# Performance work log

Hardware: AMD Instinct MI355X
Metric: run time of the kernel (lower is better)

## Reference

```python
import jax, jax.numpy as jnp
import numpy as np

H = 64
L = 3
NG = 1024
# node types: 0 user, 1 card, 2 transaction, 3 merchant, 4 location, 5 device
N_NODES = [100000, 150000, 500000, 20000, 5000, 50000]
N_TX = N_NODES[2]
FEAT_DIMS = [8, 6, 12, 6, 5, 5]
NAMES = ["user", "card", "transaction", "merchant", "location", "device"]
# relation r -> (src_type, dst_type); order matches the HeteroConv dict:
# owns, made, at, in, using, followed_by, owned_by, made_with, receives, has, used_in, preceded
REL = [(0, 1), (1, 2), (2, 3), (2, 4), (2, 5), (2, 2), (1, 0), (2, 1), (3, 2), (4, 2), (5, 2), (2, 2)]
E_CNT = [150000, 500000, 500000, 500000, 500000, 500000, 150000, 500000, 500000, 500000, 500000, 500000]


def gat_conv(x_src, x_dst, src, dst, W, a_s, a_d, b, n_dst):
    # PyG GATConv, heads=1, shared src/dst linear (int in_channels), no self-loops (bipartite hetero)
    xs = x_src @ W  # [Ns, H]
    xd = x_dst @ W  # [Nd, H]
    e = jax.nn.leaky_relu((xs @ a_s)[src] + (xd @ a_d)[dst], 0.2)  # [E]
    m = jax.ops.segment_max(e, dst, num_segments=n_dst)
    m = jnp.where(jnp.isfinite(m), m, 0.0)
    p = jnp.exp(e - m[dst])
    s = jax.ops.segment_sum(p, dst, num_segments=n_dst)
    alpha = p / (s[dst] + 1e-16)
    out = jax.ops.segment_sum(alpha[:, None] * xs[src], dst, num_segments=n_dst)
    return out + b


def setup_inputs():
    key = jax.random.key(0)
    ks = iter(jax.random.split(key, 80))
    inp = {}
    for n, d, nm in zip(N_NODES, FEAT_DIMS, NAMES):
        inp["x_" + nm] = jax.random.normal(next(ks), (n, d), jnp.float32)
    for d, nm in zip(FEAT_DIMS, NAMES):
        inp["emb_" + nm + "_W"] = (jax.random.normal(next(ks), (d, H), jnp.float32) / np.sqrt(d)).astype(jnp.float32)
        inp["emb_" + nm + "_b"] = jnp.zeros((H,), jnp.float32)
    inp["gat_W"] = (jax.random.normal(next(ks), (L, 12, H, H), jnp.float32) / np.sqrt(H)).astype(jnp.float32)
    inp["gat_a_src"] = jax.random.normal(next(ks), (L, 12, H), jnp.float32) * 0.1
    inp["gat_a_dst"] = jax.random.normal(next(ks), (L, 12, H), jnp.float32) * 0.1
    inp["gat_b"] = jnp.zeros((L, 12, H), jnp.float32)
    inp["pool_W"] = (jax.random.normal(next(ks), (2 * H, H), jnp.float32) / np.sqrt(2 * H)).astype(jnp.float32)
    inp["pool_b"] = jnp.zeros((H,), jnp.float32)
    inp["cls_W1"] = (jax.random.normal(next(ks), (H, H), jnp.float32) / np.sqrt(H)).astype(jnp.float32)
    inp["cls_b1"] = jnp.zeros((H,), jnp.float32)
    inp["cls_W2"] = (jax.random.normal(next(ks), (H, 1), jnp.float32) / np.sqrt(H)).astype(jnp.float32)
    inp["cls_b2"] = jnp.zeros((1,), jnp.float32)
    for r, (s, d) in enumerate(REL):
        inp[f"e{r}_src"] = jax.random.randint(next(ks), (E_CNT[r],), 0, N_NODES[s])
        inp[f"e{r}_dst"] = jax.random.randint(next(ks), (E_CNT[r],), 0, N_NODES[d])
    inp["batch"] = jnp.sort(jax.random.randint(next(ks), (N_TX,), 0, NG))
    return inp


def reference(x_user, x_card, x_transaction, x_merchant, x_location, x_device,
              emb_user_W, emb_user_b, emb_card_W, emb_card_b,
              emb_transaction_W, emb_transaction_b, emb_merchant_W, emb_merchant_b,
              emb_location_W, emb_location_b, emb_device_W, emb_device_b,
              gat_W, gat_a_src, gat_a_dst, gat_b,
              pool_W, pool_b, cls_W1, cls_b1, cls_W2, cls_b2,
              e0_src, e0_dst, e1_src, e1_dst, e2_src, e2_dst, e3_src, e3_dst,
              e4_src, e4_dst, e5_src, e5_dst, e6_src, e6_dst, e7_src, e7_dst,
              e8_src, e8_dst, e9_src, e9_dst, e10_src, e10_dst, e11_src, e11_dst,
              batch):
    edges = [(e0_src, e0_dst), (e1_src, e1_dst), (e2_src, e2_dst), (e3_src, e3_dst),
             (e4_src, e4_dst), (e5_src, e5_dst), (e6_src, e6_dst), (e7_src, e7_dst),
             (e8_src, e8_dst), (e9_src, e9_dst), (e10_src, e10_dst), (e11_src, e11_dst)]
    x = [x_user @ emb_user_W + emb_user_b,
         x_card @ emb_card_W + emb_card_b,
         x_transaction @ emb_transaction_W + emb_transaction_b,
         x_merchant @ emb_merchant_W + emb_merchant_b,
         x_location @ emb_location_W + emb_location_b,
         x_device @ emb_device_W + emb_device_b]
    for l in range(L):
        agg = [jnp.zeros((n, H), x[0].dtype) for n in N_NODES]
        for r, (s, d) in enumerate(REL):  # HeteroConv default aggr='sum'
            agg[d] = agg[d] + gat_conv(x[s], x[d], edges[r][0], edges[r][1],
                                       gat_W[l, r], gat_a_src[l, r], gat_a_dst[l, r],
                                       gat_b[l, r], N_NODES[d])
        x = [jax.nn.relu(a) for a in agg]  # dropout(p=0.2) is identity in eval mode
    tx = x[2]
    cnt = jax.ops.segment_sum(jnp.ones((N_TX,), tx.dtype), batch, num_segments=NG)
    mean_pool = jax.ops.segment_sum(tx, batch, num_segments=NG) / jnp.maximum(cnt, 1.0)[:, None]
    max_pool = jax.ops.segment_max(tx, batch, num_segments=NG)
    max_pool = jnp.where(jnp.isfinite(max_pool), max_pool, 0.0)
    pooled = jnp.concatenate([mean_pool, max_pool], axis=1) @ pool_W + pool_b
    h = jax.nn.relu(tx @ cls_W1 + cls_b1)
    fraud_scores = jax.nn.sigmoid(h @ cls_W2 + cls_b2)
    return fraud_scores, pooled
```

## Files before the change

### kernel.cpp

```cpp
#include <hip/hip_runtime.h>
#include <hip/hip_bf16.h>

typedef unsigned int u32;
typedef unsigned short u16;
typedef _Float16 f16;
typedef float f32x4 __attribute__((ext_vector_type(4)));
typedef short bf16x8 __attribute__((ext_vector_type(8)));

#define CDIV(a,b) (((a)+(b)-1)/(b))

__device__ __forceinline__ float bf2f(u32 h){ return __uint_as_float(h<<16); }
__device__ __forceinline__ u16 f2bf(float f){
  u32 u=__float_as_uint(f);
  return (u16)((u + 0x7fffu + ((u>>16)&1u))>>16);
}
__device__ __forceinline__ void unpack8(const u16* p, float* xr){
  uint4 v=*(const uint4*)p;
  xr[0]=bf2f(v.x&0xffffu); xr[1]=bf2f(v.x>>16);
  xr[2]=bf2f(v.y&0xffffu); xr[3]=bf2f(v.y>>16);
  xr[4]=bf2f(v.z&0xffffu); xr[5]=bf2f(v.z>>16);
  xr[6]=bf2f(v.w&0xffffu); xr[7]=bf2f(v.w>>16);
}
__device__ __forceinline__ int iclamp(int i, int n){
  unsigned u=(unsigned)i; return (u>=(unsigned)n)?0:i;
}

struct EdgeTab {
  const int* dst[12];
  const int* src[12];
  int seo[13];
  int rpo[13];
  int nd[12];
  int ns[12];
};

struct GTab {
  int nn[6]; int xo[6];
  int rst[12];
  int aso[12], ado[12], rpo[12], seo[12];
  int tord[6]; int bofs[7];
  int abofs[7];
  int nrel[6], rel[6][6];
  int nrole[6]; int rwv[6][12]; int rofs[6][12];
  int dszb;
};

__global__ void kdiag(float* out, int n, float v){
  int i=blockIdx.x*blockDim.x+threadIdx.x;
  if(i<n) out[i]=(i==0)?v:0.f;
}
__global__ void kzeroi(int* p, int n){
  int i=blockIdx.x*blockDim.x+threadIdx.x;
  if(i<n) p[i]=0;
}
__global__ void kbsum(const float* __restrict__ gb, float* __restrict__ bsum){
  int l=blockIdx.x/6, t=blockIdx.x%6, j=threadIdx.x;
  const int rd[12]={1,2,3,4,5,2,0,1,2,2,2,2};
  float a=0.f;
  #pragma unroll
  for(int r=0;r<12;++r) if(rd[r]==t) a += gb[(l*12+r)*64 + j];
  bsum[(l*6+t)*64 + j]=a;
}
__global__ void kwconv(const float* __restrict__ gw, u16* __restrict__ wt, int total){
  int o=blockIdx.x*blockDim.x+threadIdx.x;
  if(o>=total) return;
  int m=o>>12, rem=o&4095, j=rem>>6, k=rem&63;
  wt[o]=f2bf(gw[(m<<12)+(k<<6)+j]);
}
__global__ void kwv(const float* __restrict__ gw, const float* __restrict__ gas,
                    const float* __restrict__ gad, float* __restrict__ wv){
  int m=blockIdx.x;
  int lr=m>>1, role=m&1;
  int k=threadIdx.x;
  const float* a=(role?gad:gas)+(size_t)lr*64;
  const float* W=gw+(size_t)lr*4096;
  float acc=0.f;
  for(int j=0;j<64;++j) acc += W[k*64+j]*a[j];
  wv[(size_t)m*64+k]=acc;
}

__global__ void khistC(EdgeTab et, int* __restrict__ RP, int Etot, int c0, int c1){
  int i=blockIdx.x*blockDim.x+threadIdx.x;
  if(i>=Etot) return;
  int r=0;
  #pragma unroll
  for(int k=1;k<12;++k) r += (i>=et.seo[k]) ? 1 : 0;
  int e=i-et.seo[r];
  int rpidx=et.rpo[r]+iclamp(et.dst[r][e], et.nd[r]);
  if(rpidx>=c0 && rpidx<c1) atomicAdd(RP+rpidx,1);
}
__global__ void kscan1(const int* __restrict__ hist, int* __restrict__ rp, int* __restrict__ bsum, int N){
  __shared__ int lds[256];
  __shared__ int pref[256];
  int b=blockIdx.x, t=threadIdx.x;
  int base=b*4096+t*16;
  int v[16]; int s=0;
  #pragma unroll
  for(int k=0;k<16;++k){ int idx=base+k; v[k]=(idx<N)?hist[idx]:0; s+=v[k]; }
  lds[t]=s; __syncthreads();
  if(t==0){ int run=0; for(int i=0;i<256;++i){ pref[i]=run; run+=lds[i]; } bsum[b]=run; }
  __syncthreads();
  int run=pref[t];
  #pragma unroll
  for(int k=0;k<16;++k){ int idx=base+k; if(idx<N) rp[idx]=run; run+=v[k]; }
}
__global__ void kscan2b(int* bsum, int nb){
  __shared__ int lds[256], pref[256], tot;
  int t=threadIdx.x;
  int v[4]; int s=0;
  #pragma unroll
  for(int k=0;k<4;++k){ int idx=t*4+k; v[k]=(idx<nb)?bsum[idx]:0; s+=v[k]; }
  lds[t]=s; __syncthreads();
  if(t==0){ int run=0; for(int i=0;i<256;++i){ pref[i]=run; run+=lds[i]; } tot=run; }
  __syncthreads();
  int run=pref[t];
  #pragma unroll
  for(int k=0;k<4;++k){ int idx=t*4+k; if(idx<nb){ int x=v[k]; bsum[idx]=run; run+=x; } }
  if(t==0) bsum[nb]=tot;
}
__global__ void kscan3(int* __restrict__ rp, const int* __restrict__ bsum, int N){
  int i=blockIdx.x*blockDim.x+threadIdx.x;
  if(i<N) rp[i]+=bsum[i>>12];
}
__global__ void kscatterC(EdgeTab et, int* __restrict__ RP, int* __restrict__ SRCS,
                          int Etot, int c0, int c1){
  int i=blockIdx.x*blockDim.x+threadIdx.x;
  if(i>=Etot) return;
  int r=0;
  #pragma unroll
  for(int k=1;k<12;++k) r += (i>=et.seo[k]) ? 1 : 0;
  int e=i-et.seo[r];
  int rpidx=et.rpo[r]+iclamp(et.dst[r][e], et.nd[r]);
  if(rpidx>=c0 && rpidx<c1){
    int pos=atomicAdd(RP+rpidx,1);
    SRCS[pos]=iclamp(et.src[r][e], et.ns[r]);
  }
}

template<int D>
__global__ void kemb(const float* __restrict__ xin, const float* __restrict__ W,
                     const float* __restrict__ b, u16* __restrict__ xout, int N,
                     const float* __restrict__ WV0, f16* __restrict__ AA, GTab tab, int t){
  int n=blockIdx.x*blockDim.x+threadIdx.x;
  if(n>=N) return;
  float xr[D];
  #pragma unroll
  for(int k=0;k<D;++k) xr[k]=xin[(long)n*D+k];
  float o[64];
  u16* orow=xout+(long)n*64;
  #pragma unroll
  for(int j0=0;j0<64;j0+=8){
    #pragma unroll
    for(int jj=0;jj<8;++jj){
      float a=b[j0+jj];
      #pragma unroll
      for(int k=0;k<D;++k) a += xr[k]*W[k*64+j0+jj];
      o[j0+jj]=a;
    }
    uint4 pk;
    pk.x=(u32)f2bf(o[j0+0])|((u32)f2bf(o[j0+1])<<16);
    pk.y=(u32)f2bf(o[j0+2])|((u32)f2bf(o[j0+3])<<16);
    pk.z=(u32)f2bf(o[j0+4])|((u32)f2bf(o[j0+5])<<16);
    pk.w=(u32)f2bf(o[j0+6])|((u32)f2bf(o[j0+7])<<16);
    *(uint4*)(orow+j0)=pk;
  }
  int nr=tab.nrole[t];
  for(int ro=0;ro<nr;++ro){
    const float* wv=WV0+(size_t)tab.rwv[t][ro]*64;
    float acc=0.f;
    #pragma unroll
    for(int k=0;k<64;++k) acc += o[k]*wv[k];
    AA[tab.rofs[t][ro]+n]=(f16)acc;
  }
}

__global__ void kalphaM(const u16* __restrict__ X, const float* __restrict__ WVl,
                        f16* __restrict__ AA, GTab tab){
  __shared__ float wv[12*64];
  int b=blockIdx.x, tid=threadIdx.x;
  int ti=0;
  #pragma unroll
  for(int k=1;k<6;++k) ti += (b>=tab.abofs[k]) ? 1 : 0;
  int t=tab.tord[ti];
  int nr=tab.nrole[t];
  for(int i=tid;i<nr*64;i+=256){
    int ro=i>>6, j=i&63;
    wv[i]=WVl[tab.rwv[t][ro]*64+j];
  }
  __syncthreads();
  int nid=(b-tab.abofs[ti])*256+tid;
  if(nid>=tab.nn[t]) return;
  const u16* row=X+((long)tab.xo[t]+nid)*64;
  float xr[64];
  #pragma unroll
  for(int j=0;j<64;j+=8) unpack8(row+j,xr+j);
  for(int ro=0;ro<nr;++ro){
    float acc=0.f;
    #pragma unroll
    for(int k=0;k<64;++k) acc += xr[k]*wv[ro*64+k];
    AA[tab.rofs[t][ro]+nid]=(f16)acc;
  }
}

#define LZ 0
#define LW 8192
__global__ void kfusedM2(const u16* __restrict__ Xc, u16* __restrict__ Xn,
                         const u16* __restrict__ WTl, const f16* __restrict__ AA,
                         const int* __restrict__ RP, const int* __restrict__ SRCS,
                         const float* __restrict__ BSl, GTab tab){
  __shared__ char L[16384];
  int tid=threadIdx.x;
  int b=blockIdx.x;
  int ti=0;
  #pragma unroll
  for(int k=1;k<6;++k) ti += (b>=tab.bofs[k]) ? 1 : 0;
  int t=tab.tord[ti];
  int d0=(b-tab.bofs[ti])*64;
  int Nt=tab.nn[t];
  int nid=tid>>2, q=tid&3;
  int d=d0+nid;

  f32x4 acc[4];
  #pragma unroll
  for(int ct=0;ct<4;++ct){ acc[ct][0]=0.f; acc[ct][1]=0.f; acc[ct][2]=0.f; acc[ct][3]=0.f; }

  int nrel=tab.nrel[t];
  for(int ri=0;ri<nrel;++ri){
    int r=tab.rel[t][ri];
    __syncthreads();
    {
      const uint4* s4=(const uint4*)(WTl+(size_t)r*4096);
      uint4 v0=s4[tid*2], v1=s4[tid*2+1];
      int b0=tid*32, j=b0>>7;
      *(uint4*)(L+LW+((b0   )^((j&7)<<4)))=v0;
      *(uint4*)(L+LW+((b0+16)^((j&7)<<4)))=v1;
    }
    float z[16];
    #pragma unroll
    for(int k=0;k<16;++k) z[k]=0.f;
    float sden=0.f;
    if(d<Nt){
      int b1=RP[tab.rpo[r]+d];
      int b0e= d? RP[tab.rpo[r]+d-1] : tab.seo[r];
      float adv=(float)AA[tab.dszb+tab.ado[r]+d];
      const u16* xbase=Xc+(long)tab.xo[tab.rst[r]]*64;
      const f16* asp=AA+tab.aso[r];
      float m=-3.4e38f;
      for(int e=b0e;e<b1;++e){
        float ev=(float)asp[SRCS[e]]+adv;
        ev = ev>=0.f?ev:0.2f*ev;
        m=fmaxf(m,ev);
      }
      int e=b0e;
      for(; e+1<b1; e+=2){
        int sr0=SRCS[e], sr1=SRCS[e+1];
        float ev0=(float)asp[sr0]+adv; ev0 = ev0>=0.f?ev0:0.2f*ev0;
        float ev1=(float)asp[sr1]+adv; ev1 = ev1>=0.f?ev1:0.2f*ev1;
        float p0=__expf(ev0-m), p1=__expf(ev1-m);
        const u16* rw0=xbase+(long)sr0*64+q*16;
        const u16* rw1=xbase+(long)sr1*64+q*16;
        uint4 a0=*(const uint4*)rw0;
        uint4 a1=*(const uint4*)(rw0+8);
        uint4 c0=*(const uint4*)rw1;
        uint4 c1=*(const uint4*)(rw1+8);
        sden+=p0+p1;
        float xr[8];
        unpack8((const u16*)&a0,xr);
        #pragma unroll
        for(int k=0;k<8;++k) z[k]+=p0*xr[k];
        unpack8((const u16*)&a1,xr);
        #pragma unroll
        for(int k=0;k<8;++k) z[8+k]+=p0*xr[k];
        unpack8((const u16*)&c0,xr);
        #pragma unroll
        for(int k=0;k<8;++k) z[k]+=p1*xr[k];
        unpack8((const u16*)&c1,xr);
        #pragma unroll
        for(int k=0;k<8;++k) z[8+k]+=p1*xr[k];
      }
      if(e<b1){
        int sr0=SRCS[e];
        float ev0=(float)asp[sr0]+adv; ev0 = ev0>=0.f?ev0:0.2f*ev0;
        float p0=__expf(ev0-m);
        const u16* rw0=xbase+(long)sr0*64+q*16;
        uint4 a0=*(const uint4*)rw0;
        uint4 a1=*(const uint4*)(rw0+8);
        sden+=p0;
        float xr[8];
        unpack8((const u16*)&a0,xr);
        #pragma unroll
        for(int k=0;k<8;++k) z[k]+=p0*xr[k];
        unpack8((const u16*)&a1,xr);
        #pragma unroll
        for(int k=0;k<8;++k) z[8+k]+=p0*xr[k];
      }
    }
    float inv=1.f/(sden+1e-16f);
    {
      uint4 p0,p1;
      p0.x=(u32)f2bf(z[0]*inv) |((u32)f2bf(z[1]*inv)<<16);
      p0.y=(u32)f2bf(z[2]*inv) |((u32)f2bf(z[3]*inv)<<16);
      p0.z=(u32)f2bf(z[4]*inv) |((u32)f2bf(z[5]*inv)<<16);
      p0.w=(u32)f2bf(z[6]*inv) |((u32)f2bf(z[7]*inv)<<16);
      p1.x=(u32)f2bf(z[8]*inv) |((u32)f2bf(z[9]*inv)<<16);
      p1.y=(u32)f2bf(z[10]*inv)|((u32)f2bf(z[11]*inv)<<16);
      p1.z=(u32)f2bf(z[12]*inv)|((u32)f2bf(z[13]*inv)<<16);
      p1.w=(u32)f2bf(z[14]*inv)|((u32)f2bf(z[15]*inv)<<16);
      int zb=nid*128+q*32;
      *(uint4*)(L+LZ+((zb   )^((nid&7)<<4)))=p0;
      *(uint4*)(L+LZ+((zb+16)^((nid&7)<<4)))=p1;
    }
    __syncthreads();
    {
      int w=tid>>6, l=tid&63;
      int nt=w*16;
      int arow=nt+(l&15);
      int kb=(l>>4)*8;
      #pragma unroll
      for(int ks=0;ks<64;ks+=32){
        int ab=arow*128+(ks+kb)*2;
        uint4 av=*(uint4*)(L+LZ+(ab^((arow&7)<<4)));
        bf16x8 af=*(bf16x8*)&av;
        #pragma unroll
        for(int ct=0;ct<4;++ct){
          int jrow=ct*16+(l&15);
          int bb=jrow*128+(ks+kb)*2;
          uint4 bv=*(uint4*)(L+LW+(bb^((jrow&7)<<4)));
          bf16x8 bfr=*(bf16x8*)&bv;
          acc[ct]=__builtin_amdgcn_mfma_f32_16x16x32_bf16(af,bfr,acc[ct],0,0,0);
        }
      }
    }
  }
  __syncthreads();
  {
    int w=tid>>6, l=tid&63;
    int nt=w*16;
    #pragma unroll
    for(int ct=0;ct<4;++ct){
      #pragma unroll
      for(int r4=0;r4<4;++r4){
        int crow=nt+(l>>4)*4+r4;
        int ccol=ct*16+(l&15);
        int cb=crow*256+ccol*4;
        *(float*)(L+(cb^((crow&7)<<4)))=acc[ct][r4];
      }
    }
  }
  __syncthreads();
  {
    int nn=tid>>2, cq=tid&3;
    if(d0+nn<Nt){
      float cv[16];
      #pragma unroll
      for(int p=0;p<4;++p){
        int cb=nn*256+cq*64+p*16;
        uint4 v=*(uint4*)(L+(cb^((nn&7)<<4)));
        const float* f=(const float*)&v;
        cv[p*4+0]=f[0]; cv[p*4+1]=f[1]; cv[p*4+2]=f[2]; cv[p*4+3]=f[3];
      }
      const float* bs=BSl+t*64+cq*16;
      u32 wd[8];
      #pragma unroll
      for(int i=0;i<8;++i){
        float lo=fmaxf(cv[2*i]  +bs[2*i],  0.f);
        float hi=fmaxf(cv[2*i+1]+bs[2*i+1],0.f);
        wd[i]=(u32)f2bf(lo)|((u32)f2bf(hi)<<16);
      }
      u16* orow=Xn+((long)tab.xo[t]+d0+nn)*64+cq*16;
      uint4 s0; s0.x=wd[0]; s0.y=wd[1]; s0.z=wd[2]; s0.w=wd[3];
      uint4 s1; s1.x=wd[4]; s1.y=wd[5]; s1.z=wd[6]; s1.w=wd[7];
      *(uint4*)orow=s0;
      *(uint4*)(orow+8)=s1;
    }
  }
}

__global__ void kcls(const u16* __restrict__ tx, const float* __restrict__ W1,
                     const float* __restrict__ b1, const float* __restrict__ W2,
                     const float* __restrict__ b2, float* __restrict__ out, int N){
  int n=blockIdx.x*blockDim.x+threadIdx.x;
  if(n>=N) return;
  const u16* row=tx+(long)n*64;
  float xr[64];
  #pragma unroll
  for(int j=0;j<64;j+=8) unpack8(row+j,xr+j);
  float acc2=0.f;
  for(int j=0;j<64;++j){
    float a=b1[j];
    #pragma unroll
    for(int k=0;k<64;++k) a += xr[k]*W1[k*64+j];
    a=fmaxf(a,0.f);
    acc2 += a*W2[j];
  }
  float zv=acc2+b2[0];
  out[n]=1.f/(1.f+__expf(-zv));
}

__global__ void kgrp(const int* __restrict__ batch, int* __restrict__ grp, int N){
  int g=blockIdx.x*blockDim.x+threadIdx.x;
  if(g>1024) return;
  if(g==1024){ grp[1024]=N; return; }
  int lo=0, hi=N;
  while(lo<hi){ int mid=(lo+hi)>>1; if(batch[mid]<g) lo=mid+1; else hi=mid; }
  grp[g]=lo;
}
__global__ void kpoolf(const u16* __restrict__ tx, const int* __restrict__ grp,
                       const float* __restrict__ pW, const float* __restrict__ pb,
                       float* __restrict__ out){
  __shared__ float S[256], M[256], V[128];
  int g=blockIdx.x, t=threadIdx.x, w=t>>6, j=t&63;
  int n0=grp[g], n1=grp[g+1];
  float s=0.f, m=-3.4e38f;
  for(int n=n0+w; n<n1; n+=4){
    float v=bf2f(tx[(long)n*64+j]);
    s+=v; m=fmaxf(m,v);
  }
  S[t]=s; M[t]=m; __syncthreads();
  if(t<64){
    float ss=S[t]+S[t+64]+S[t+128]+S[t+192];
    float mm=fmaxf(fmaxf(M[t],M[t+64]),fmaxf(M[t+128],M[t+192]));
    int cnt=n1-n0;
    V[t]=ss/fmaxf((float)cnt,1.f);
    V[64+t]=(cnt>0)?mm:0.f;
  }
  __syncthreads();
  if(t<64){
    float acc=pb[t];
    for(int k=0;k<128;++k) acc+=V[k]*pW[k*64+t];
    out[(long)g*64+t]=acc;
  }
}

extern "C" void kernel_launch(void* const* d_in, const int* in_sizes, int n_in,
                              void* d_out, int out_size, void* d_ws, size_t ws_size,
                              hipStream_t stream){
  const int   NN[6]={100000,150000,500000,20000,5000,50000};
  const long  XO[6]={0,100000,250000,750000,770000,775000};
  const int   RS[12]={0,1,2,2,2,2,1,2,3,4,5,2};
  const int   RD[12]={1,2,3,4,5,2,0,1,2,2,2,2};
  const int   EC[12]={150000,500000,500000,500000,500000,500000,150000,500000,500000,500000,500000,500000};

  const float* xin[6];  for(int t=0;t<6;++t) xin[t]=(const float*)d_in[t];
  const float* embW[6]; const float* embB[6];
  for(int t=0;t<6;++t){ embW[t]=(const float*)d_in[6+2*t]; embB[t]=(const float*)d_in[7+2*t]; }
  const float* gatW =(const float*)d_in[18];
  const float* gatAs=(const float*)d_in[19];
  const float* gatAd=(const float*)d_in[20];
  const float* gatB =(const float*)d_in[21];
  const float* poolW=(const float*)d_in[22];
  const float* poolB=(const float*)d_in[23];
  const float* W1=(const float*)d_in[24];
  const float* b1=(const float*)d_in[25];
  const float* W2=(const float*)d_in[26];
  const float* b2=(const float*)d_in[27];
  const int* esrc[12]; const int* edst[12];
  for(int r=0;r<12;++r){ esrc[r]=(const int*)d_in[28+2*r]; edst[r]=(const int*)d_in[29+2*r]; }
  const int* batch=(const int*)d_in[52];
  float* out=(float*)d_out;
  (void)in_sizes; (void)n_in;

  EdgeTab et;
  GTab tab;
  int rpo=0, seo=0, asz=0, dsz=0;
  for(int r=0;r<12;++r){
    et.dst[r]=edst[r]; et.src[r]=esrc[r];
    et.seo[r]=seo; et.rpo[r]=rpo;
    et.nd[r]=NN[RD[r]]; et.ns[r]=NN[RS[r]];
    tab.rst[r]=RS[r];
    tab.seo[r]=seo; tab.rpo[r]=rpo;
    tab.aso[r]=asz; tab.ado[r]=dsz;
    seo+=EC[r]; rpo+=NN[RD[r]]+1;
    asz+=NN[RS[r]]; dsz+=NN[RD[r]];
  }
  et.seo[12]=seo; et.rpo[12]=rpo;
  const int Etot=seo;
  const int RPtot=rpo;
  tab.dszb=asz;
  for(int t=0;t<6;++t){ tab.nn[t]=NN[t]; tab.xo[t]=(int)XO[t]; }
  const int TORD[6]={4,3,5,2,1,0};
  int bo=0, abo=0;
  for(int i=0;i<6;++i){
    int t=TORD[i];
    tab.tord[i]=t;
    tab.bofs[i]=bo;   bo+=CDIV(NN[t],64);
    tab.abofs[i]=abo; abo+=CDIV(NN[t],256);
  }
  tab.bofs[6]=bo; tab.abofs[6]=abo;
  for(int t=0;t<6;++t){ tab.nrel[t]=0; tab.nrole[t]=0; }
  for(int r=0;r<12;++r){
    int dt=RD[r];
    tab.rel[dt][tab.nrel[dt]++]=r;
    int st=RS[r];
    tab.rwv[st][tab.nrole[st]]=r*2+0;   tab.rofs[st][tab.nrole[st]++]=tab.aso[r];
    tab.rwv[dt][tab.nrole[dt]]=r*2+1;   tab.rofs[dt][tab.nrole[dt]++]=asz+tab.ado[r];
  }

  char* w=(char*)d_ws;
  size_t off=0;
  auto take=[&](size_t bytes)->void*{
    void* p=w+off; off+=(bytes+(size_t)255)&~(size_t)255; return p;
  };
  u16*   X1   =(u16*)  take(105600000);
  u16*   X2   =(u16*)  take(105600000);
  int*   RP   =(int*)  take((size_t)RPtot*4);
  int*   SRCS =(int*)  take((size_t)Etot*4);
  int*   BS   =(int*)  take(4096);
  f16*   AA   =(f16*)  take((size_t)(asz+dsz)*2);
  float* WV   =(float*)take(72*64*4);
  float* BSUM =(float*)take(4608);
  int*   GRP  =(int*)  take(4104);
  u16*   WT   =(u16*)  take(294912);
  size_t need=off;

  const int B=256;

  if(ws_size<need){
    kdiag<<<CDIV(out_size,B),B,0,stream>>>(out,out_size,(float)(ws_size>>20));
    return;
  }

  kwconv<<<CDIV(147456,B),B,0,stream>>>(gatW,WT,147456);
  kwv<<<72,64,0,stream>>>(gatW,gatAs,gatAd,WV);
  kbsum<<<18,64,0,stream>>>(gatB,BSUM);

  const int NCH=8;
  int CS=CDIV(RPtot,NCH);
  kzeroi<<<CDIV(RPtot,B),B,0,stream>>>(RP,RPtot);
  for(int c=0;c<NCH;++c){
    int c0=c*CS, c1=min(RPtot,c0+CS);
    khistC<<<CDIV(Etot,B),B,0,stream>>>(et,RP,Etot,c0,c1);
  }
  int nbs=CDIV(RPtot,4096);
  kscan1<<<nbs,256,0,stream>>>(RP,RP,BS,RPtot);
  kscan2b<<<1,256,0,stream>>>(BS,nbs);
  kscan3<<<CDIV(RPtot,B),B,0,stream>>>(RP,BS,RPtot);
  for(int c=0;c<NCH;++c){
    int c0=c*CS, c1=min(RPtot,c0+CS);
    kscatterC<<<CDIV(Etot,B),B,0,stream>>>(et,RP,SRCS,Etot,c0,c1);
  }

  kemb< 8><<<CDIV(NN[0],B),B,0,stream>>>(xin[0],embW[0],embB[0],X1+XO[0]*64,NN[0],WV,AA,tab,0);
  kemb< 6><<<CDIV(NN[1],B),B,0,stream>>>(xin[1],embW[1],embB[1],X1+XO[1]*64,NN[1],WV,AA,tab,1);
  kemb<12><<<CDIV(NN[2],B),B,0,stream>>>(xin[2],embW[2],embB[2],X1+XO[2]*64,NN[2],WV,AA,tab,2);
  kemb< 6><<<CDIV(NN[3],B),B,0,stream>>>(xin[3],embW[3],embB[3],X1+XO[3]*64,NN[3],WV,AA,tab,3);
  kemb< 5><<<CDIV(NN[4],B),B,0,stream>>>(xin[4],embW[4],embB[4],X1+XO[4]*64,NN[4],WV,AA,tab,4);
  kemb< 5><<<CDIV(NN[5],B),B,0,stream>>>(xin[5],embW[5],embB[5],X1+XO[5]*64,NN[5],WV,AA,tab,5);

  u16* Xc=X1; u16* Xn=X2;
  for(int l=0;l<3;++l){
    if(l>0) kalphaM<<<abo,256,0,stream>>>(Xc,WV+(size_t)l*1536,AA,tab);
    kfusedM2<<<bo,256,0,stream>>>(Xc,Xn,WT+(size_t)l*49152,AA,RP,SRCS,
                                  BSUM+(size_t)l*384,tab);
    u16* tmp=Xc; Xc=Xn; Xn=tmp;
  }

  kcls<<<CDIV(NN[2],B),B,0,stream>>>(Xc+XO[2]*64,W1,b1,W2,b2,out,NN[2]);

  kgrp<<<CDIV(1025,B),B,0,stream>>>(batch,GRP,NN[2]);
  kpoolf<<<1024,256,0,stream>>>(Xc+XO[2]*64,GRP,poolW,poolB,out+500000);
}
```

Before: 2.506 ms.

## Replace per-destination softmax max pass with a global per-relation upper bound

The GAT softmax no longer scans each destination's edges once just to find the max logit. Instead, kemb and kalphaM use wave reductions and atomicMax on order-preserving encoded floats to record the global max of the source and destination attention terms per relation. kfusedM2 turns the sum of those two maxima into a shared shift through leaky-ReLU. This removes one gather pass over SRCS and the attention array per relation, at the cost of a few extra atomics. Because softmax is shift-invariant the result is mathematically unchanged, but if logits span a wide range, exp could underflow for destinations whose logits sit far below the global bound.

```diff
diff --git a/kernel.cpp b/kernel.cpp
--- a/kernel.cpp
+++ b/kernel.cpp
@@ -13,6 +13,14 @@
 __device__ __forceinline__ u16 f2bf(float f){
   u32 u=__float_as_uint(f);
   return (u16)((u + 0x7fffu + ((u>>16)&1u))>>16);
+}
+__device__ __forceinline__ u32 fenc(float f){
+  u32 u=__float_as_uint(f);
+  return (u&0x80000000u)?~u:(u|0x80000000u);
+}
+__device__ __forceinline__ float fdec2(u32 e){
+  u32 u=(e&0x80000000u)?(e&0x7fffffffu):~e;
+  return __uint_as_float(u);
 }
 __device__ __forceinline__ void unpack8(const u16* p, float* xr){
   uint4 v=*(const uint4*)p;
@@ -140,14 +148,15 @@
 template<int D>
 __global__ void kemb(const float* __restrict__ xin, const float* __restrict__ W,
                      const float* __restrict__ b, u16* __restrict__ xout, int N,
-                     const float* __restrict__ WV0, f16* __restrict__ AA, GTab tab, int t){
+                     const float* __restrict__ WV0, f16* __restrict__ AA,
+                     u32* __restrict__ MG0, GTab tab, int t){
   int n=blockIdx.x*blockDim.x+threadIdx.x;
-  if(n>=N) return;
+  bool valid=(n<N);
+  int nc=valid?n:0;
   float xr[D];
   #pragma unroll
-  for(int k=0;k<D;++k) xr[k]=xin[(long)n*D+k];
+  for(int k=0;k<D;++k) xr[k]=xin[(long)nc*D+k];
   float o[64];
-  u16* orow=xout+(long)n*64;
   #pragma unroll
   for(int j0=0;j0<64;j0+=8){
     #pragma unroll
@@ -157,12 +166,14 @@
       for(int k=0;k<D;++k) a += xr[k]*W[k*64+j0+jj];
       o[j0+jj]=a;
     }
-    uint4 pk;
-    pk.x=(u32)f2bf(o[j0+0])|((u32)f2bf(o[j0+1])<<16);
-    pk.y=(u32)f2bf(o[j0+2])|((u32)f2bf(o[j0+3])<<16);
-    pk.z=(u32)f2bf(o[j0+4])|((u32)f2bf(o[j0+5])<<16);
-    pk.w=(u32)f2bf(o[j0+6])|((u32)f2bf(o[j0+7])<<16);
-    *(uint4*)(orow+j0)=pk;
+    if(valid){
+      uint4 pk;
+      pk.x=(u32)f2bf(o[j0+0])|((u32)f2bf(o[j0+1])<<16);
+      pk.y=(u32)f2bf(o[j0+2])|((u32)f2bf(o[j0+3])<<16);
+      pk.z=(u32)f2bf(o[j0+4])|((u32)f2bf(o[j0+5])<<16);
+      pk.w=(u32)f2bf(o[j0+6])|((u32)f2bf(o[j0+7])<<16);
+      *(uint4*)(xout+(long)n*64+j0)=pk;
+    }
   }
   int nr=tab.nrole[t];
   for(int ro=0;ro<nr;++ro){
@@ -170,12 +181,16 @@
     float acc=0.f;
     #pragma unroll
     for(int k=0;k<64;++k) acc += o[k]*wv[k];
-    AA[tab.rofs[t][ro]+n]=(f16)acc;
+    if(valid) AA[tab.rofs[t][ro]+n]=(f16)acc;
+    float mx=valid?acc:-3.4e38f;
+    #pragma unroll
+    for(int off=32;off;off>>=1) mx=fmaxf(mx,__shfl_xor(mx,off));
+    if((threadIdx.x&63)==0) atomicMax(MG0+tab.rwv[t][ro],fenc(mx));
   }
 }
 
 __global__ void kalphaM(const u16* __restrict__ X, const float* __restrict__ WVl,
-                        f16* __restrict__ AA, GTab tab){
+                        f16* __restrict__ AA, u32* __restrict__ MGl, GTab tab){
   __shared__ float wv[12*64];
   int b=blockIdx.x, tid=threadIdx.x;
   int ti=0;
@@ -189,8 +204,9 @@
   }
   __syncthreads();
   int nid=(b-tab.abofs[ti])*256+tid;
-  if(nid>=tab.nn[t]) return;
-  const u16* row=X+((long)tab.xo[t]+nid)*64;
+  bool valid=(nid<tab.nn[t]);
+  int nc=valid?nid:0;
+  const u16* row=X+((long)tab.xo[t]+nc)*64;
   float xr[64];
   #pragma unroll
   for(int j=0;j<64;j+=8) unpack8(row+j,xr+j);
@@ -198,7 +214,11 @@
     float acc=0.f;
     #pragma unroll
     for(int k=0;k<64;++k) acc += xr[k]*wv[ro*64+k];
-    AA[tab.rofs[t][ro]+nid]=(f16)acc;
+    if(valid) AA[tab.rofs[t][ro]+nid]=(f16)acc;
+    float mx=valid?acc:-3.4e38f;
+    #pragma unroll
+    for(int off=32;off;off>>=1) mx=fmaxf(mx,__shfl_xor(mx,off));
+    if((tid&63)==0) atomicMax(MGl+tab.rwv[t][ro],fenc(mx));
   }
 }
 
@@ -207,7 +227,8 @@
 __global__ void kfusedM2(const u16* __restrict__ Xc, u16* __restrict__ Xn,
                          const u16* __restrict__ WTl, const f16* __restrict__ AA,
                          const int* __restrict__ RP, const int* __restrict__ SRCS,
-                         const float* __restrict__ BSl, GTab tab){
+                         const float* __restrict__ BSl, const u32* __restrict__ MGl,
+                         GTab tab){
   __shared__ char L[16384];
   int tid=threadIdx.x;
   int b=blockIdx.x;
@@ -227,6 +248,8 @@
   int nrel=tab.nrel[t];
   for(int ri=0;ri<nrel;++ri){
     int r=tab.rel[t][ri];
+    float msum=fdec2(MGl[r*2])+fdec2(MGl[r*2+1]);
+    float m = msum>=0.f? msum : 0.2f*msum;
     __syncthreads();
     {
       const uint4* s4=(const uint4*)(WTl+(size_t)r*4096);
@@ -245,12 +268,6 @@
       float adv=(float)AA[tab.dszb+tab.ado[r]+d];
       const u16* xbase=Xc+(long)tab.xo[tab.rst[r]]*64;
       const f16* asp=AA+tab.aso[r];
-      float m=-3.4e38f;
-      for(int e=b0e;e<b1;++e){
-        float ev=(float)asp[SRCS[e]]+adv;
-        ev = ev>=0.f?ev:0.2f*ev;
-        m=fmaxf(m,ev);
-      }
       int e=b0e;
       for(; e+1<b1; e+=2){
         int sr0=SRCS[e], sr1=SRCS[e+1];
@@ -511,6 +528,7 @@
   float* BSUM =(float*)take(4608);
   int*   GRP  =(int*)  take(4104);
   u16*   WT   =(u16*)  take(294912);
+  u32*   MG   =(u32*)  take(288);
   size_t need=off;
 
   const int B=256;
@@ -523,6 +541,7 @@
   kwconv<<<CDIV(147456,B),B,0,stream>>>(gatW,WT,147456);
   kwv<<<72,64,0,stream>>>(gatW,gatAs,gatAd,WV);
   kbsum<<<18,64,0,stream>>>(gatB,BSUM);
+  kzeroi<<<1,72,0,stream>>>((int*)MG,72);
 
   const int NCH=8;
   int CS=CDIV(RPtot,NCH);
@@ -540,18 +559,18 @@
     kscatterC<<<CDIV(Etot,B),B,0,stream>>>(et,RP,SRCS,Etot,c0,c1);
   }
 
-  kemb< 8><<<CDIV(NN[0],B),B,0,stream>>>(xin[0],embW[0],embB[0],X1+XO[0]*64,NN[0],WV,AA,tab,0);
-  kemb< 6><<<CDIV(NN[1],B),B,0,stream>>>(xin[1],embW[1],embB[1],X1+XO[1]*64,NN[1],WV,AA,tab,1);
-  kemb<12><<<CDIV(NN[2],B),B,0,stream>>>(xin[2],embW[2],embB[2],X1+XO[2]*64,NN[2],WV,AA,tab,2);
-  kemb< 6><<<CDIV(NN[3],B),B,0,stream>>>(xin[3],embW[3],embB[3],X1+XO[3]*64,NN[3],WV,AA,tab,3);
-  kemb< 5><<<CDIV(NN[4],B),B,0,stream>>>(xin[4],embW[4],embB[4],X1+XO[4]*64,NN[4],WV,AA,tab,4);
-  kemb< 5><<<CDIV(NN[5],B),B,0,stream>>>(xin[5],embW[5],embB[5],X1+XO[5]*64,NN[5],WV,AA,tab,5);
+  kemb< 8><<<CDIV(NN[0],B),B,0,stream>>>(xin[0],embW[0],embB[0],X1+XO[0]*64,NN[0],WV,AA,MG,tab,0);
+  kemb< 6><<<CDIV(NN[1],B),B,0,stream>>>(xin[1],embW[1],embB[1],X1+XO[1]*64,NN[1],WV,AA,MG,tab,1);
+  kemb<12><<<CDIV(NN[2],B),B,0,stream>>>(xin[2],embW[2],embB[2],X1+XO[2]*64,NN[2],WV,AA,MG,tab,2);
+  kemb< 6><<<CDIV(NN[3],B),B,0,stream>>>(xin[3],embW[3],embB[3],X1+XO[3]*64,NN[3],WV,AA,MG,tab,3);
+  kemb< 5><<<CDIV(NN[4],B),B,0,stream>>>(xin[4],embW[4],embB[4],X1+XO[4]*64,NN[4],WV,AA,MG,tab,4);
+  kemb< 5><<<CDIV(NN[5],B),B,0,stream>>>(xin[5],embW[5],embB[5],X1+XO[5]*64,NN[5],WV,AA,MG,tab,5);
 
   u16* Xc=X1; u16* Xn=X2;
   for(int l=0;l<3;++l){
-    if(l>0) kalphaM<<<abo,256,0,stream>>>(Xc,WV+(size_t)l*1536,AA,tab);
+    if(l>0) kalphaM<<<abo,256,0,stream>>>(Xc,WV+(size_t)l*1536,AA,MG+(size_t)l*24,tab);
     kfusedM2<<<bo,256,0,stream>>>(Xc,Xn,WT+(size_t)l*49152,AA,RP,SRCS,
-                                  BSUM+(size_t)l*384,tab);
+                                  BSUM+(size_t)l*384,MG+(size_t)l*24,tab);
     u16* tmp=Xc; Xc=Xn; Xn=tmp;
   }
 
```

Result: slower. 4.176 ms (+66.7%).

## Replace per-destination softmax max pass with global per-relation max bound

Applied to the files above, without the earlier changes.

Adds a small kernel that computes, per layer and relation, the global maximum of the source and destination attention logits. It encodes floats as order-preserving integers so a single atomicMax works. The fused aggregation kernel then uses leaky_relu(max_src + max_dst) as the softmax shift instead of first walking every incoming edge to find the exact segment max. This removes one full gather pass over the edge list and the source logits per relation. The shift relies on softmax being shift-invariant, but a loose global bound risks exp underflow, and so lost precision or a zero denominator, when logits spread widely.

```diff
diff --git a/kernel.cpp b/kernel.cpp
--- a/kernel.cpp
+++ b/kernel.cpp
@@ -13,6 +13,14 @@
 __device__ __forceinline__ u16 f2bf(float f){
   u32 u=__float_as_uint(f);
   return (u16)((u + 0x7fffu + ((u>>16)&1u))>>16);
+}
+__device__ __forceinline__ u32 fenc(float f){
+  u32 u=__float_as_uint(f);
+  return (u&0x80000000u)?~u:(u|0x80000000u);
+}
+__device__ __forceinline__ float fdec2(u32 e){
+  u32 u=(e&0x80000000u)?(e&0x7fffffffu):~e;
+  return __uint_as_float(u);
 }
 __device__ __forceinline__ void unpack8(const u16* p, float* xr){
   uint4 v=*(const uint4*)p;
@@ -36,7 +44,7 @@
 
 struct GTab {
   int nn[6]; int xo[6];
-  int rst[12];
+  int rst[12]; int rdt[12];
   int aso[12], ado[12], rpo[12], seo[12];
   int tord[6]; int bofs[7];
   int abofs[7];
@@ -202,12 +210,35 @@
   }
 }
 
+__global__ void kmg(const f16* __restrict__ AA, u32* __restrict__ MGl, GTab tab){
+  const int NB=8;
+  int b=blockIdx.x;
+  int ro=b/NB, part=b%NB;
+  int r=ro>>1, role=ro&1;
+  int base,len;
+  if(role==0){ base=tab.aso[r];           len=tab.nn[tab.rst[r]]; }
+  else       { base=tab.dszb+tab.ado[r];  len=tab.nn[tab.rdt[r]]; }
+  int i0=(int)((long)len*part/NB), i1=(int)((long)len*(part+1)/NB);
+  float m=-3.4e38f;
+  for(int i=i0+threadIdx.x;i<i1;i+=256) m=fmaxf(m,(float)AA[base+i]);
+  #pragma unroll
+  for(int off=32;off;off>>=1) m=fmaxf(m,__shfl_xor(m,off));
+  __shared__ float red[4];
+  if((threadIdx.x&63)==0) red[threadIdx.x>>6]=m;
+  __syncthreads();
+  if(threadIdx.x==0){
+    float mm=fmaxf(fmaxf(red[0],red[1]),fmaxf(red[2],red[3]));
+    atomicMax(MGl+ro,fenc(mm));
+  }
+}
+
 #define LZ 0
 #define LW 8192
 __global__ void kfusedM2(const u16* __restrict__ Xc, u16* __restrict__ Xn,
                          const u16* __restrict__ WTl, const f16* __restrict__ AA,
                          const int* __restrict__ RP, const int* __restrict__ SRCS,
-                         const float* __restrict__ BSl, GTab tab){
+                         const float* __restrict__ BSl, const u32* __restrict__ MGl,
+                         GTab tab){
   __shared__ char L[16384];
   int tid=threadIdx.x;
   int b=blockIdx.x;
@@ -227,6 +258,8 @@
   int nrel=tab.nrel[t];
   for(int ri=0;ri<nrel;++ri){
     int r=tab.rel[t][ri];
+    float msum=fdec2(MGl[r*2])+fdec2(MGl[r*2+1]);
+    float m = msum>=0.f? msum : 0.2f*msum;
     __syncthreads();
     {
       const uint4* s4=(const uint4*)(WTl+(size_t)r*4096);
@@ -245,12 +278,6 @@
       float adv=(float)AA[tab.dszb+tab.ado[r]+d];
       const u16* xbase=Xc+(long)tab.xo[tab.rst[r]]*64;
       const f16* asp=AA+tab.aso[r];
-      float m=-3.4e38f;
-      for(int e=b0e;e<b1;++e){
-        float ev=(float)asp[SRCS[e]]+adv;
-        ev = ev>=0.f?ev:0.2f*ev;
-        m=fmaxf(m,ev);
-      }
       int e=b0e;
       for(; e+1<b1; e+=2){
         int sr0=SRCS[e], sr1=SRCS[e+1];
@@ -467,7 +494,7 @@
     et.dst[r]=edst[r]; et.src[r]=esrc[r];
     et.seo[r]=seo; et.rpo[r]=rpo;
     et.nd[r]=NN[RD[r]]; et.ns[r]=NN[RS[r]];
-    tab.rst[r]=RS[r];
+    tab.rst[r]=RS[r]; tab.rdt[r]=RD[r];
     tab.seo[r]=seo; tab.rpo[r]=rpo;
     tab.aso[r]=asz; tab.ado[r]=dsz;
     seo+=EC[r]; rpo+=NN[RD[r]]+1;
@@ -511,6 +538,7 @@
   float* BSUM =(float*)take(4608);
   int*   GRP  =(int*)  take(4104);
   u16*   WT   =(u16*)  take(294912);
+  u32*   MG   =(u32*)  take(288);
   size_t need=off;
 
   const int B=256;
@@ -523,6 +551,7 @@
   kwconv<<<CDIV(147456,B),B,0,stream>>>(gatW,WT,147456);
   kwv<<<72,64,0,stream>>>(gatW,gatAs,gatAd,WV);
   kbsum<<<18,64,0,stream>>>(gatB,BSUM);
+  kzeroi<<<1,72,0,stream>>>((int*)MG,72);
 
   const int NCH=8;
   int CS=CDIV(RPtot,NCH);
@@ -550,8 +579,9 @@
   u16* Xc=X1; u16* Xn=X2;
   for(int l=0;l<3;++l){
     if(l>0) kalphaM<<<abo,256,0,stream>>>(Xc,WV+(size_t)l*1536,AA,tab);
+    kmg<<<24*8,256,0,stream>>>(AA,MG+(size_t)l*24,tab);
     kfusedM2<<<bo,256,0,stream>>>(Xc,Xn,WT+(size_t)l*49152,AA,RP,SRCS,
-                                  BSUM+(size_t)l*384,tab);
+                                  BSUM+(size_t)l*384,MG+(size_t)l*24,tab);
     u16* tmp=Xc; Xc=Xn; Xn=tmp;
   }
 
```

Measured after the change: 2.344 ms. 6.5% less time.
